# Kernel optimization log

Hardware: AMD Instinct MI355X
Metric: run time of the kernel (lower is better)

## Reference

```python
import jax, jax.numpy as jnp
import numpy as np

NUM_SEGMENTS = 65536   # number of token groups (output rows)
TOTAL_TOKENS = 1048576 # total rows across all ragged groups (~16 per group)
D = 128                # per-token feature width


def setup_inputs() -> dict:
    rng = np.random.default_rng(0)
    # every segment gets >= 1 token; distribute the rest randomly
    extra = rng.multinomial(TOTAL_TOKENS - NUM_SEGMENTS,
                            np.full(NUM_SEGMENTS, 1.0 / NUM_SEGMENTS))
    lengths = 1 + extra
    offsets = np.concatenate([[0], np.cumsum(lengths)[:-1]]).astype(np.int32)
    segment_ids = np.repeat(np.arange(NUM_SEGMENTS, dtype=np.int32), lengths)
    key = jax.random.key(0)
    values = jax.random.normal(key, (TOTAL_TOKENS, D), dtype=jnp.float32)
    return {
        "values": values,
        "segment_ids": jnp.asarray(segment_ids),
        "offsets": jnp.asarray(offsets),
    }


def reference(values, segment_ids, offsets):
    # values: [T, D]; segment_ids: [T] sorted; offsets: [S] start index of each group
    S = offsets.shape[0]
    sums = jax.ops.segment_sum(values, segment_ids, num_segments=S)          # [S, D]
    counts = jax.ops.segment_sum(jnp.ones((values.shape[0], 1), values.dtype),
                                 segment_ids, num_segments=S)                 # [S, 1]
    mean = sums / counts                                                      # torch.mean(token, dim=0)
    mx = jax.ops.segment_max(values, segment_ids, num_segments=S)             # torch.max(token, dim=0).values
    first = values[offsets]                                                   # token[0, :]
    return jnp.concatenate([first, mean, mx], axis=1)                         # [S, 3*D]
```

## Files before the change

kernel.cpp:

```cpp
#include <hip/hip_runtime.h>


constexpr int NSEG = 65536;
constexpr int NTOK = 1048576;
constexpr int D    = 128;

__global__ __launch_bounds__(256) void token_feat_kernel(
    const float* __restrict__ values,
    const int*   __restrict__ offsets,
    float*       __restrict__ out)
{
    const int gid  = blockIdx.x * blockDim.x + threadIdx.x;
    const int seg  = gid >> 6;
    const int lane = gid & 63;
    if (seg >= NSEG) return;

    const int start = offsets[seg];
    const int end   = (seg + 1 < NSEG) ? offsets[seg + 1] : NTOK;
    const int L     = end - start;

    const float2* __restrict__ base =
        reinterpret_cast<const float2*>(values) + (size_t)start * (D / 2) + lane;

    float2 v = base[0];
    const float2 first = v;
    float sx = v.x, sy = v.y;
    float mx = v.x, my = v.y;

    for (int t = 1; t < L; ++t) {
        const float2 w = base[(size_t)t * (D / 2)];
        sx += w.x;  sy += w.y;
        mx = fmaxf(mx, w.x);  my = fmaxf(my, w.y);
    }

    const float inv = 1.0f / (float)L;

    float2* __restrict__ o = reinterpret_cast<float2*>(out) + (size_t)seg * (3 * D / 2);
    o[lane]       = first;
    o[64 + lane]  = make_float2(sx * inv, sy * inv);
    o[128 + lane] = make_float2(mx, my);
}

extern "C" void kernel_launch(void* const* d_in, const int* in_sizes, int n_in,
                              void* d_out, int out_size, void* d_ws, size_t ws_size,
                              hipStream_t stream) {
    const float* values  = (const float*)d_in[0];
    const int*   offsets = (const int*)d_in[2];
    float*       out     = (float*)d_out;

    const int threads       = 256;
    const int wavesPerBlock = threads / 64;
    const int blocks        = (NSEG + wavesPerBlock - 1) / wavesPerBlock;
    token_feat_kernel<<<blocks, threads, 0, stream>>>(values, offsets, out);
}
```

Before: 138.9 us.

## Use 16-byte loads with two rows per wave and unrolled accumulation

Each wave now reads float4 vectors, with the two half-waves handling alternating rows. The main loop is unrolled by eight rows, issuing four independent loads per thread, and the halves are merged with cross-lane shuffles. Outputs go out as nontemporal vector stores. The aim is more memory-level parallelism and fewer, wider memory instructions in a bandwidth-bound kernel, at the cost of extra shuffles and a remainder loop for short segments.

```diff
diff --git a/kernel.cpp b/kernel.cpp
--- a/kernel.cpp
+++ b/kernel.cpp
@@ -1,14 +1,18 @@
 #include <hip/hip_runtime.h>
+#include <float.h>
 
+
+typedef float f32x4 __attribute__((ext_vector_type(4)));
 
 constexpr int NSEG = 65536;
 constexpr int NTOK = 1048576;
 constexpr int D    = 128;
+constexpr int D4   = D / 4;
 
 __global__ __launch_bounds__(256) void token_feat_kernel(
-    const float* __restrict__ values,
+    const f32x4* __restrict__ v4,
     const int*   __restrict__ offsets,
-    float*       __restrict__ out)
+    f32x4*       __restrict__ out4)
 {
     const int gid  = blockIdx.x * blockDim.x + threadIdx.x;
     const int seg  = gid >> 6;
@@ -19,37 +23,65 @@
     const int end   = (seg + 1 < NSEG) ? offsets[seg + 1] : NTOK;
     const int L     = end - start;
 
-    const float2* __restrict__ base =
-        reinterpret_cast<const float2*>(values) + (size_t)start * (D / 2) + lane;
+    const int c = lane & 31;
+    const int h = lane >> 5;
 
-    float2 v = base[0];
-    const float2 first = v;
-    float sx = v.x, sy = v.y;
-    float mx = v.x, my = v.y;
+    const f32x4* __restrict__ base = v4 + (size_t)start * D4 + c;
 
-    for (int t = 1; t < L; ++t) {
-        const float2 w = base[(size_t)t * (D / 2)];
-        sx += w.x;  sy += w.y;
-        mx = fmaxf(mx, w.x);  my = fmaxf(my, w.y);
+    f32x4 sum   = (f32x4){0.f, 0.f, 0.f, 0.f};
+    f32x4 mx    = (f32x4){-FLT_MAX, -FLT_MAX, -FLT_MAX, -FLT_MAX};
+    f32x4 first = (f32x4){0.f, 0.f, 0.f, 0.f};
+
+    int r0 = 0;
+    for (; r0 + 8 <= L; r0 += 8) {
+        const f32x4 w0 = base[(size_t)(r0 + 0 + h) * D4];
+        const f32x4 w1 = base[(size_t)(r0 + 2 + h) * D4];
+        const f32x4 w2 = base[(size_t)(r0 + 4 + h) * D4];
+        const f32x4 w3 = base[(size_t)(r0 + 6 + h) * D4];
+        if (r0 == 0) first = w0;
+        sum += w0 + w1 + w2 + w3;
+        mx.x = fmaxf(fmaxf(fmaxf(mx.x, w0.x), fmaxf(w1.x, w2.x)), w3.x);
+        mx.y = fmaxf(fmaxf(fmaxf(mx.y, w0.y), fmaxf(w1.y, w2.y)), w3.y);
+        mx.z = fmaxf(fmaxf(fmaxf(mx.z, w0.z), fmaxf(w1.z, w2.z)), w3.z);
+        mx.w = fmaxf(fmaxf(fmaxf(mx.w, w0.w), fmaxf(w1.w, w2.w)), w3.w);
+    }
+    for (int r = r0 + h; r < L; r += 2) {
+        const f32x4 w = base[(size_t)r * D4];
+        if (r == 0) first = w;
+        sum += w;
+        mx.x = fmaxf(mx.x, w.x);  mx.y = fmaxf(mx.y, w.y);
+        mx.z = fmaxf(mx.z, w.z);  mx.w = fmaxf(mx.w, w.w);
     }
 
+    sum.x += __shfl_xor(sum.x, 32);
+    sum.y += __shfl_xor(sum.y, 32);
+    sum.z += __shfl_xor(sum.z, 32);
+    sum.w += __shfl_xor(sum.w, 32);
+    mx.x = fmaxf(mx.x, __shfl_xor(mx.x, 32));
+    mx.y = fmaxf(mx.y, __shfl_xor(mx.y, 32));
+    mx.z = fmaxf(mx.z, __shfl_xor(mx.z, 32));
+    mx.w = fmaxf(mx.w, __shfl_xor(mx.w, 32));
+
     const float inv = 1.0f / (float)L;
+    const f32x4 mean = sum * inv;
 
-    float2* __restrict__ o = reinterpret_cast<float2*>(out) + (size_t)seg * (3 * D / 2);
-    o[lane]       = first;
-    o[64 + lane]  = make_float2(sx * inv, sy * inv);
-    o[128 + lane] = make_float2(mx, my);
+    f32x4* __restrict__ o = out4 + (size_t)seg * 96;
+    if (lane < 32) {
+        __builtin_nontemporal_store(first, o + c);
+    }
+    const f32x4 mm = (lane < 32) ? mean : mx;
+    __builtin_nontemporal_store(mm, o + 32 + lane);
 }
 
 extern "C" void kernel_launch(void* const* d_in, const int* in_sizes, int n_in,
                               void* d_out, int out_size, void* d_ws, size_t ws_size,
                               hipStream_t stream) {
-    const float* values  = (const float*)d_in[0];
+    const f32x4* values  = (const f32x4*)d_in[0];
     const int*   offsets = (const int*)d_in[2];
-    float*       out     = (float*)d_out;
+    f32x4*       out     = (f32x4*)d_out;
 
     const int threads       = 256;
     const int wavesPerBlock = threads / 64;
-    const int blocks        = (NSEG + wavesPerBlock - 1) / wavesPerBlock;
+    const int blocks        = NSEG / wavesPerBlock;
     token_feat_kernel<<<blocks, threads, 0, stream>>>(values, offsets, out);
 }
```

Result: faster. 119.0 us (-14.3%).
